# Kernel tuning notes

Hardware: AMD Instinct MI355X
Metric: run time of the kernel (lower is better)

Reference implementation:

```python
import jax, jax.numpy as jnp
import numpy as np

G = 8          # grid_size
DH = 32        # dim_head
EPS = 1e-5
INIT_LS = 1e-5


def setup_inputs() -> dict:
    key = jax.random.key(0)
    ks = jax.random.split(key, 8)
    B, H, W, C = 16, 128, 128, 256
    s = 1.0 / np.sqrt(C)
    return {
        "x": jax.random.normal(ks[0], (B, H, W, C), dtype=jnp.float32),
        "ln_w": jnp.ones((C,), jnp.float32),
        "ln_b": jnp.zeros((C,), jnp.float32),
        "in_proj_w": jax.random.uniform(ks[1], (3 * C, C), jnp.float32, -s, s),
        "in_proj_b": jnp.zeros((3 * C,), jnp.float32),
        "out_proj_w": jax.random.uniform(ks[2], (C, C), jnp.float32, -s, s),
        "out_proj_b": jnp.zeros((C,), jnp.float32),
        "gamma": jnp.full((C,), INIT_LS, jnp.float32),
    }


def _grid_attention(x, ln_w, ln_b, in_proj_w, in_proj_b, out_proj_w, out_proj_b, gamma):
    B, H, W, C = x.shape
    nh = C // DH
    # LayerNorm over channels
    mu = jnp.mean(x, axis=-1, keepdims=True)
    var = jnp.mean(jnp.square(x - mu), axis=-1, keepdims=True)
    x = (x - mu) * jax.lax.rsqrt(var + EPS) * ln_w + ln_b
    # grid partition: (B,G,H/G,G,W/G,C) -> (B,H/G,W/G,G,G,C) -> (N, G*G, C)
    hg, wg = H // G, W // G
    xw = x.reshape(B, G, hg, G, wg, C).transpose(0, 2, 4, 1, 3, 5)
    xw = xw.reshape(B * hg * wg, G * G, C)  # N windows of L=G*G tokens
    # MHSA (nn.MultiheadAttention semantics)
    qkv = xw @ in_proj_w.T + in_proj_b                      # (N, L, 3C)
    q, k, v = jnp.split(qkv, 3, axis=-1)
    N, L = xw.shape[0], xw.shape[1]
    q = q.reshape(N, L, nh, DH).transpose(0, 2, 1, 3)        # (N, nh, L, DH)
    k = k.reshape(N, L, nh, DH).transpose(0, 2, 1, 3)
    v = v.reshape(N, L, nh, DH).transpose(0, 2, 1, 3)
    scores = jnp.einsum("nhld,nhmd->nhlm", q, k) / np.sqrt(DH)
    attn = jax.nn.softmax(scores, axis=-1)
    out = jnp.einsum("nhlm,nhmd->nhld", attn, v)             # (N, nh, L, DH)
    out = out.transpose(0, 2, 1, 3).reshape(N, L, C)
    out = out @ out_proj_w.T + out_proj_b
    # LayerScale
    out = out * gamma
    # grid reverse: (B,H/G,W/G,G,G,C) -> (B,G,H/G,G,W/G,C) -> (B,H,W,C)
    out = out.reshape(B, hg, wg, G, G, C).transpose(0, 3, 1, 4, 2, 5)
    return out.reshape(B, H, W, C)


def reference(x, ln_w, ln_b, in_proj_w, in_proj_b, out_proj_w, out_proj_b, gamma):
    return _grid_attention(x, ln_w, ln_b, in_proj_w, in_proj_b,
                           out_proj_w, out_proj_b, gamma)
```

## Files before the change

kernel.cpp:

```cpp
#include <hip/hip_runtime.h>
#include <hip/hip_bf16.h>

typedef __attribute__((ext_vector_type(8))) short short8;
typedef __attribute__((ext_vector_type(4))) float f32x4;
typedef __attribute__((ext_vector_type(4))) unsigned short us4;
typedef __attribute__((ext_vector_type(2))) unsigned uint2v;

union U8 { unsigned u[4]; short8 s; };

__device__ __forceinline__ unsigned short f2b(float f) {
  unsigned u = __float_as_uint(f);
  u += 0x7FFFu + ((u >> 16) & 1u);
  return (unsigned short)(u >> 16);
}
__device__ __forceinline__ float b2f(unsigned short h) {
  return __uint_as_float((unsigned)h << 16);
}
__device__ __forceinline__ unsigned pkbf(float lo, float hi) {
  __hip_bfloat162 h = __float22bfloat162_rn(make_float2(lo, hi));
  unsigned u; __builtin_memcpy(&u, &h, 4);
  return u;
}
__device__ __forceinline__ void swp32(unsigned &a, unsigned &b) {
#if __has_builtin(__builtin_amdgcn_permlane32_swap)
  uint2v r = __builtin_amdgcn_permlane32_swap(a, b, false, false);
  a = r.x; b = r.y;
#else
  asm volatile("v_permlane32_swap_b32 %0, %1" : "+v"(a), "+v"(b));
#endif
}
__device__ __forceinline__ void swp16(unsigned &a, unsigned &b) {
#if __has_builtin(__builtin_amdgcn_permlane16_swap)
  uint2v r = __builtin_amdgcn_permlane16_swap(a, b, false, false);
  a = r.x; b = r.y;
#else
  asm volatile("v_permlane16_swap_b32 %0, %1" : "+v"(a), "+v"(b));
#endif
}

__global__ __launch_bounds__(64) void prep(
    const float* __restrict__ wq, const float* __restrict__ wo,
    const float* __restrict__ lnw, const float* __restrict__ lnb,
    const float* __restrict__ bqkv, const float* __restrict__ bo,
    const float* __restrict__ gm,
    unsigned short* __restrict__ wbf, float* __restrict__ Sarr,
    float* __restrict__ Carr, float* __restrict__ boG) {
  int d = blockIdx.x, lane = threadIdx.x;
  if (d < 768) {
    float4 wv = *(const float4*)(wq + (size_t)d * 256 + lane * 4);
    float4 lw = *(const float4*)(lnw + lane * 4);
    float4 lb = *(const float4*)(lnb + lane * 4);
    us4 o;
    o.x = f2b(wv.x * lw.x); o.y = f2b(wv.y * lw.y);
    o.z = f2b(wv.z * lw.z); o.w = f2b(wv.w * lw.w);
    *(us4*)(wbf + (size_t)d * 256 + lane * 4) = o;
    float s = b2f(o.x) + b2f(o.y) + b2f(o.z) + b2f(o.w);
    float c = wv.x * lb.x + wv.y * lb.y + wv.z * lb.z + wv.w * lb.w;
    #pragma unroll
    for (int m = 32; m >= 1; m >>= 1) { s += __shfl_xor(s, m); c += __shfl_xor(c, m); }
    if (lane == 0) { Sarr[d] = s; Carr[d] = c + bqkv[d]; }
  } else {
    int dd = d - 768;
    float g = gm[dd];
    float4 wv = *(const float4*)(wo + (size_t)dd * 256 + lane * 4);
    us4 o;
    o.x = f2b(wv.x * g); o.y = f2b(wv.y * g); o.z = f2b(wv.z * g); o.w = f2b(wv.w * g);
    *(us4*)(wbf + 196608 + (size_t)dd * 256 + lane * 4) = o;
    if (lane == 0) boG[dd] = bo[dd] * g;
  }
}

__global__ __launch_bounds__(512, 4) void grid_attn(
    const float* __restrict__ x,
    const unsigned short* __restrict__ Wqkv,
    const unsigned short* __restrict__ Wout,
    const float* __restrict__ Sarr,
    const float* __restrict__ Carr,
    const float* __restrict__ boG,
    float* __restrict__ out) {

  __shared__ unsigned short ldsX[64 * 264];
  __shared__ float ldsMu[64];
  __shared__ float ldsRs[64];

  const int tid = threadIdx.x;
  const int w   = tid >> 6;
  const int lid = tid & 63;
  const int l16 = lid & 15;
  const int lhi = lid >> 4;

  const int n  = blockIdx.x;
  const int b  = n >> 8;
  const int wi = (n >> 4) & 15;
  const int wj = n & 15;

  {
    float2 p[8];
    #pragma unroll
    for (int t = 0; t < 8; ++t) {
      int l = w * 8 + t;
      int a = l >> 3, cg = l & 7;
      int hh = a * 16 + wi, ww = cg * 16 + wj;
      float4 v = *(const float4*)(x + ((size_t)((b * 128 + hh) * 128 + ww)) * 256 + lid * 4);
      p[t].x = v.x + v.y + v.z + v.w;
      p[t].y = v.x * v.x + v.y * v.y + v.z * v.z + v.w * v.w;
      uint2v o; o.x = pkbf(v.x, v.y); o.y = pkbf(v.z, v.w);
      *(uint2v*)(&ldsX[l * 264 + lid * 4]) = o;
    }
    const int h1 = lid & 1, h2 = (lid >> 1) & 1, h4 = (lid >> 2) & 1;
    float2 q[4];
    #pragma unroll
    for (int i = 0; i < 4; ++i) {
      float sx = h1 ? p[i].x : p[i + 4].x, sy = h1 ? p[i].y : p[i + 4].y;
      float kx = h1 ? p[i + 4].x : p[i].x, ky = h1 ? p[i + 4].y : p[i].y;
      q[i].x = kx + __shfl_xor(sx, 1);
      q[i].y = ky + __shfl_xor(sy, 1);
    }
    float2 r2[2];
    #pragma unroll
    for (int i = 0; i < 2; ++i) {
      float sx = h2 ? q[i].x : q[i + 2].x, sy = h2 ? q[i].y : q[i + 2].y;
      float kx = h2 ? q[i + 2].x : q[i].x, ky = h2 ? q[i + 2].y : q[i].y;
      r2[i].x = kx + __shfl_xor(sx, 2);
      r2[i].y = ky + __shfl_xor(sy, 2);
    }
    float fx, fy;
    {
      float sx = h4 ? r2[0].x : r2[1].x, sy = h4 ? r2[0].y : r2[1].y;
      float kx = h4 ? r2[1].x : r2[0].x, ky = h4 ? r2[1].y : r2[0].y;
      fx = kx + __shfl_xor(sx, 4);
      fy = ky + __shfl_xor(sy, 4);
    }
    fx += __shfl_xor(fx, 8);  fy += __shfl_xor(fy, 8);
    fx += __shfl_xor(fx, 16); fy += __shfl_xor(fy, 16);
    fx += __shfl_xor(fx, 32); fy += __shfl_xor(fy, 32);
    if (lid < 8) {
      int T = h1 * 4 + h2 * 2 + h4;
      float mu = fx * (1.0f / 256.0f);
      float var = fy * (1.0f / 256.0f) - mu * mu;
      ldsMu[w * 8 + T] = mu;
      ldsRs[w * 8 + T] = rsqrtf(var + 1e-5f);
    }
  }
  __syncthreads();

  short8 vtf[2][2];
  {
    f32x4 va[4][2];
    #pragma unroll
    for (int tt = 0; tt < 4; ++tt)
      #pragma unroll
      for (int dt = 0; dt < 2; ++dt)
        va[tt][dt] = (f32x4){0.f, 0.f, 0.f, 0.f};
    const unsigned short* wvp = Wqkv + (size_t)(512 + w * 32 + l16) * 256 + lhi * 8;
    #pragma unroll 4
    for (int kc = 0; kc < 8; ++kc) {
      short8 wv0 = *(const short8*)(wvp + kc * 32);
      short8 wv1 = *(const short8*)(wvp + 16 * 256 + kc * 32);
      #pragma unroll
      for (int tt = 0; tt < 4; ++tt) {
        short8 xf = *(const short8*)(&ldsX[(tt * 16 + l16) * 264 + kc * 32 + lhi * 8]);
        va[tt][0] = __builtin_amdgcn_mfma_f32_16x16x32_bf16(xf, wv0, va[tt][0], 0, 0, 0);
        va[tt][1] = __builtin_amdgcn_mfma_f32_16x16x32_bf16(xf, wv1, va[tt][1], 0, 0, 0);
      }
    }
    #pragma unroll
    for (int dt = 0; dt < 2; ++dt) {
      float Sv = Sarr[512 + w * 32 + dt * 16 + l16];
      float Cv = Carr[512 + w * 32 + dt * 16 + l16];
      unsigned bu[8];
      #pragma unroll
      for (int tt = 0; tt < 4; ++tt) {
        f32x4 rs4 = *(const f32x4*)(&ldsRs[tt * 16 + lhi * 4]);
        f32x4 m4  = *(const f32x4*)(&ldsMu[tt * 16 + lhi * 4]);
        float v0 = fmaf(rs4[0], fmaf(-m4[0], Sv, va[tt][dt][0]), Cv);
        float v1 = fmaf(rs4[1], fmaf(-m4[1], Sv, va[tt][dt][1]), Cv);
        float v2 = fmaf(rs4[2], fmaf(-m4[2], Sv, va[tt][dt][2]), Cv);
        float v3 = fmaf(rs4[3], fmaf(-m4[3], Sv, va[tt][dt][3]), Cv);
        bu[tt * 2]     = pkbf(v0, v1);
        bu[tt * 2 + 1] = pkbf(v2, v3);
      }
      swp32(bu[0], bu[2]); swp32(bu[1], bu[3]); swp32(bu[4], bu[6]); swp32(bu[5], bu[7]);
      swp16(bu[0], bu[2]); swp16(bu[1], bu[3]); swp16(bu[4], bu[6]); swp16(bu[5], bu[7]);
      U8 z0, z1;
      z0.u[0] = bu[0]; z0.u[1] = bu[1]; z0.u[2] = bu[2]; z0.u[3] = bu[3];
      z1.u[0] = bu[4]; z1.u[1] = bu[5]; z1.u[2] = bu[6]; z1.u[3] = bu[7];
      vtf[dt][0] = z0.s;
      vtf[dt][1] = z1.s;
    }
  }

  short8 qf[4], kf[4];

  {
    f32x4 qa[2][4];
    #pragma unroll
    for (int dt = 0; dt < 2; ++dt)
      #pragma unroll
      for (int tt = 0; tt < 4; ++tt)
        qa[dt][tt] = (f32x4){0.f, 0.f, 0.f, 0.f};
    const unsigned short* wqp = Wqkv + (size_t)(w * 32 + l16) * 256 + lhi * 8;
    #pragma unroll 4
    for (int kc = 0; kc < 8; ++kc) {
      short8 wq0 = *(const short8*)(wqp + kc * 32);
      short8 wq1 = *(const short8*)(wqp + 16 * 256 + kc * 32);
      #pragma unroll
      for (int tt = 0; tt < 4; ++tt) {
        short8 xf = *(const short8*)(&ldsX[(tt * 16 + l16) * 264 + kc * 32 + lhi * 8]);
        qa[0][tt] = __builtin_amdgcn_mfma_f32_16x16x32_bf16(wq0, xf, qa[0][tt], 0, 0, 0);
        qa[1][tt] = __builtin_amdgcn_mfma_f32_16x16x32_bf16(wq1, xf, qa[1][tt], 0, 0, 0);
      }
    }
    f32x4 S0 = *(const f32x4*)(Sarr + w * 32 + lhi * 4);
    f32x4 S1 = *(const f32x4*)(Sarr + w * 32 + 16 + lhi * 4);
    f32x4 C0 = *(const f32x4*)(Carr + w * 32 + lhi * 4);
    f32x4 C1 = *(const f32x4*)(Carr + w * 32 + 16 + lhi * 4);
    #pragma unroll
    for (int tt = 0; tt < 4; ++tt) {
      float rs  = ldsRs[tt * 16 + l16];
      float nmu = -ldsMu[tt * 16 + l16];
      float e0[4], e1[4];
      #pragma unroll
      for (int r = 0; r < 4; ++r) {
        e0[r] = fmaf(rs, fmaf(nmu, S0[r], qa[0][tt][r]), C0[r]);
        e1[r] = fmaf(rs, fmaf(nmu, S1[r], qa[1][tt][r]), C1[r]);
      }
      unsigned a0 = pkbf(e0[0], e0[1]), a1 = pkbf(e0[2], e0[3]);
      unsigned a2 = pkbf(e1[0], e1[1]), a3 = pkbf(e1[2], e1[3]);
      swp32(a0, a2); swp32(a1, a3);
      swp16(a0, a2); swp16(a1, a3);
      U8 z; z.u[0] = a0; z.u[1] = a1; z.u[2] = a2; z.u[3] = a3;
      qf[tt] = z.s;
    }
  }

  {
    f32x4 ka[2][4];
    #pragma unroll
    for (int dt = 0; dt < 2; ++dt)
      #pragma unroll
      for (int tt = 0; tt < 4; ++tt)
        ka[dt][tt] = (f32x4){0.f, 0.f, 0.f, 0.f};
    const unsigned short* wkp = Wqkv + (size_t)(256 + w * 32 + l16) * 256 + lhi * 8;
    #pragma unroll 4
    for (int kc = 0; kc < 8; ++kc) {
      short8 wk0 = *(const short8*)(wkp + kc * 32);
      short8 wk1 = *(const short8*)(wkp + 16 * 256 + kc * 32);
      #pragma unroll
      for (int tt = 0; tt < 4; ++tt) {
        short8 xf = *(const short8*)(&ldsX[(tt * 16 + l16) * 264 + kc * 32 + lhi * 8]);
        ka[0][tt] = __builtin_amdgcn_mfma_f32_16x16x32_bf16(wk0, xf, ka[0][tt], 0, 0, 0);
        ka[1][tt] = __builtin_amdgcn_mfma_f32_16x16x32_bf16(wk1, xf, ka[1][tt], 0, 0, 0);
      }
    }
    f32x4 S0 = *(const f32x4*)(Sarr + 256 + w * 32 + lhi * 4);
    f32x4 S1 = *(const f32x4*)(Sarr + 256 + w * 32 + 16 + lhi * 4);
    f32x4 C0 = *(const f32x4*)(Carr + 256 + w * 32 + lhi * 4);
    f32x4 C1 = *(const f32x4*)(Carr + 256 + w * 32 + 16 + lhi * 4);
    #pragma unroll
    for (int tt = 0; tt < 4; ++tt) {
      float rs  = ldsRs[tt * 16 + l16];
      float nmu = -ldsMu[tt * 16 + l16];
      float e0[4], e1[4];
      #pragma unroll
      for (int r = 0; r < 4; ++r) {
        e0[r] = fmaf(rs, fmaf(nmu, S0[r], ka[0][tt][r]), C0[r]);
        e1[r] = fmaf(rs, fmaf(nmu, S1[r], ka[1][tt][r]), C1[r]);
      }
      unsigned a0 = pkbf(e0[0], e0[1]), a1 = pkbf(e0[2], e0[3]);
      unsigned a2 = pkbf(e1[0], e1[1]), a3 = pkbf(e1[2], e1[3]);
      swp32(a0, a2); swp32(a1, a3);
      swp16(a0, a2); swp16(a1, a3);
      U8 z; z.u[0] = a0; z.u[1] = a1; z.u[2] = a2; z.u[3] = a3;
      kf[tt] = z.s;
    }
  }

  uint2v po[4][2];
  const float K2 = 0.25503487013594137f;
  #pragma unroll
  for (int nn = 0; nn < 4; ++nn) {
    f32x4 s[4];
    #pragma unroll
    for (int m = 0; m < 4; ++m)
      s[m] = __builtin_amdgcn_mfma_f32_16x16x32_bf16(kf[m], qf[nn], (f32x4){0.f,0.f,0.f,0.f}, 0, 0, 0);
    float mx = s[0][0];
    #pragma unroll
    for (int m = 0; m < 4; ++m)
      #pragma unroll
      for (int r = 0; r < 4; ++r)
        mx = fmaxf(mx, s[m][r]);
    mx = fmaxf(mx, __shfl_xor(mx, 16));
    mx = fmaxf(mx, __shfl_xor(mx, 32));
    float sum = 0.f;
    unsigned bu[8];
    #pragma unroll
    for (int m = 0; m < 4; ++m) {
      float e0 = exp2f((s[m][0] - mx) * K2);
      float e1 = exp2f((s[m][1] - mx) * K2);
      float e2 = exp2f((s[m][2] - mx) * K2);
      float e3 = exp2f((s[m][3] - mx) * K2);
      sum += (e0 + e1) + (e2 + e3);
      bu[m * 2]     = pkbf(e0, e1);
      bu[m * 2 + 1] = pkbf(e2, e3);
    }
    sum += __shfl_xor(sum, 16);
    sum += __shfl_xor(sum, 32);
    float iv = 1.0f / sum;
    swp32(bu[0], bu[2]); swp32(bu[1], bu[3]); swp32(bu[4], bu[6]); swp32(bu[5], bu[7]);
    swp16(bu[0], bu[2]); swp16(bu[1], bu[3]); swp16(bu[4], bu[6]); swp16(bu[5], bu[7]);
    U8 z0, z1;
    z0.u[0] = bu[0]; z0.u[1] = bu[1]; z0.u[2] = bu[2]; z0.u[3] = bu[3];
    z1.u[0] = bu[4]; z1.u[1] = bu[5]; z1.u[2] = bu[6]; z1.u[3] = bu[7];
    f32x4 ot0 = (f32x4){0.f,0.f,0.f,0.f};
    f32x4 ot1 = (f32x4){0.f,0.f,0.f,0.f};
    ot0 = __builtin_amdgcn_mfma_f32_16x16x32_bf16(vtf[0][0], z0.s, ot0, 0, 0, 0);
    ot0 = __builtin_amdgcn_mfma_f32_16x16x32_bf16(vtf[0][1], z1.s, ot0, 0, 0, 0);
    ot1 = __builtin_amdgcn_mfma_f32_16x16x32_bf16(vtf[1][0], z0.s, ot1, 0, 0, 0);
    ot1 = __builtin_amdgcn_mfma_f32_16x16x32_bf16(vtf[1][1], z1.s, ot1, 0, 0, 0);
    po[nn][0].x = pkbf(ot0[0] * iv, ot0[1] * iv);
    po[nn][0].y = pkbf(ot0[2] * iv, ot0[3] * iv);
    po[nn][1].x = pkbf(ot1[0] * iv, ot1[1] * iv);
    po[nn][1].y = pkbf(ot1[2] * iv, ot1[3] * iv);
  }

  __syncthreads();

  #pragma unroll
  for (int nn = 0; nn < 4; ++nn)
    #pragma unroll
    for (int dt = 0; dt < 2; ++dt)
      *(uint2v*)(&ldsX[(nn * 16 + l16) * 264 + w * 32 + dt * 16 + lhi * 4]) = po[nn][dt];
  __syncthreads();

  f32x4 ya[4][2];
  #pragma unroll
  for (int mt = 0; mt < 4; ++mt)
    #pragma unroll
    for (int nt = 0; nt < 2; ++nt)
      ya[mt][nt] = (f32x4){0.f, 0.f, 0.f, 0.f};
  {
    const unsigned short* wop = Wout + (size_t)(w * 32 + l16) * 256 + lhi * 8;
    #pragma unroll 4
    for (int kc = 0; kc < 8; ++kc) {
      short8 wf0 = *(const short8*)(wop + kc * 32);
      short8 wf1 = *(const short8*)(wop + 16 * 256 + kc * 32);
      #pragma unroll
      for (int mt = 0; mt < 4; ++mt) {
        short8 af = *(const short8*)(&ldsX[(mt * 16 + l16) * 264 + kc * 32 + lhi * 8]);
        ya[mt][0] = __builtin_amdgcn_mfma_f32_16x16x32_bf16(af, wf0, ya[mt][0], 0, 0, 0);
        ya[mt][1] = __builtin_amdgcn_mfma_f32_16x16x32_bf16(af, wf1, ya[mt][1], 0, 0, 0);
      }
    }
  }

  float ob0 = boG[w * 32 + l16];
  float ob1 = boG[w * 32 + 16 + l16];
  #pragma unroll
  for (int mt = 0; mt < 4; ++mt)
    #pragma unroll
    for (int r = 0; r < 4; ++r) {
      int row = mt * 16 + lhi * 4 + r;
      int a = row >> 3, cg = row & 7;
      int hh = a * 16 + wi, ww2 = cg * 16 + wj;
      float* pout = out + ((size_t)((b * 128 + hh) * 128 + ww2)) * 256 + w * 32;
      pout[l16]      = ya[mt][0][r] + ob0;
      pout[l16 + 16] = ya[mt][1][r] + ob1;
    }
}

extern "C" void kernel_launch(void* const* d_in, const int* in_sizes, int n_in,
                              void* d_out, int out_size, void* d_ws, size_t ws_size,
                              hipStream_t stream) {
  const float* x    = (const float*)d_in[0];
  const float* ln_w = (const float*)d_in[1];
  const float* ln_b = (const float*)d_in[2];
  const float* ipw  = (const float*)d_in[3];
  const float* ipb  = (const float*)d_in[4];
  const float* opw  = (const float*)d_in[5];
  const float* opb  = (const float*)d_in[6];
  const float* gm   = (const float*)d_in[7];

  unsigned short* wbf = (unsigned short*)d_ws;
  float* Sarr = (float*)(wbf + 262144);
  float* Carr = Sarr + 768;
  float* boG  = Carr + 768;

  prep<<<1024, 64, 0, stream>>>(ipw, opw, ln_w, ln_b, ipb, opb, gm,
                                wbf, Sarr, Carr, boG);
  grid_attn<<<4096, 512, 0, stream>>>(x, wbf, wbf + 196608,
                                      Sarr, Carr, boG, (float*)d_out);
}
```

Before: 352.0 us.

## Apply LayerNorm before bf16 staging and seed QKV accumulators with bias

Instead of folding the LayerNorm affine into the weights and correcting each projection output with per-row mu/rstd terms, the kernel now normalizes x in registers (using ln_w/ln_b) before packing to bf16 in LDS. QKV accumulators are initialized with the in-proj bias, which removes the per-output epilogue FMAs and the S/C side arrays from the prep kernel. It also replaces shfl_xor cross-row reductions with permlane16/32 swap based reductions in LN stats and softmax. The trade-off is that the eight float4 x loads stay live in registers until the stats are ready, which raises register pressure, and precision changes slightly.

```diff
diff --git a/kernel.cpp b/kernel.cpp
--- a/kernel.cpp
+++ b/kernel.cpp
@@ -13,52 +13,46 @@
   u += 0x7FFFu + ((u >> 16) & 1u);
   return (unsigned short)(u >> 16);
 }
-__device__ __forceinline__ float b2f(unsigned short h) {
-  return __uint_as_float((unsigned)h << 16);
-}
 __device__ __forceinline__ unsigned pkbf(float lo, float hi) {
   __hip_bfloat162 h = __float22bfloat162_rn(make_float2(lo, hi));
   unsigned u; __builtin_memcpy(&u, &h, 4);
   return u;
 }
 __device__ __forceinline__ void swp32(unsigned &a, unsigned &b) {
-#if __has_builtin(__builtin_amdgcn_permlane32_swap)
   uint2v r = __builtin_amdgcn_permlane32_swap(a, b, false, false);
   a = r.x; b = r.y;
-#else
-  asm volatile("v_permlane32_swap_b32 %0, %1" : "+v"(a), "+v"(b));
-#endif
 }
 __device__ __forceinline__ void swp16(unsigned &a, unsigned &b) {
-#if __has_builtin(__builtin_amdgcn_permlane16_swap)
   uint2v r = __builtin_amdgcn_permlane16_swap(a, b, false, false);
   a = r.x; b = r.y;
-#else
-  asm volatile("v_permlane16_swap_b32 %0, %1" : "+v"(a), "+v"(b));
-#endif
+}
+__device__ __forceinline__ float redq_max(float v) {
+  uint2v r = __builtin_amdgcn_permlane16_swap(__float_as_uint(v), __float_as_uint(v), false, false);
+  v = fmaxf(__uint_as_float(r.x), __uint_as_float(r.y));
+  r = __builtin_amdgcn_permlane32_swap(__float_as_uint(v), __float_as_uint(v), false, false);
+  return fmaxf(__uint_as_float(r.x), __uint_as_float(r.y));
+}
+__device__ __forceinline__ float redq_sum(float v) {
+  uint2v r = __builtin_amdgcn_permlane16_swap(__float_as_uint(v), __float_as_uint(v), false, false);
+  v = __uint_as_float(r.x) + __uint_as_float(r.y);
+  r = __builtin_amdgcn_permlane32_swap(__float_as_uint(v), __float_as_uint(v), false, false);
+  return __uint_as_float(r.x) + __uint_as_float(r.y);
+}
+__device__ __forceinline__ float red5_sum(float v) {
+  v += __shfl_xor(v, 8);
+  return redq_sum(v);
 }
 
 __global__ __launch_bounds__(64) void prep(
     const float* __restrict__ wq, const float* __restrict__ wo,
-    const float* __restrict__ lnw, const float* __restrict__ lnb,
-    const float* __restrict__ bqkv, const float* __restrict__ bo,
-    const float* __restrict__ gm,
-    unsigned short* __restrict__ wbf, float* __restrict__ Sarr,
-    float* __restrict__ Carr, float* __restrict__ boG) {
+    const float* __restrict__ gm, const float* __restrict__ bo,
+    unsigned short* __restrict__ wbf, float* __restrict__ boG) {
   int d = blockIdx.x, lane = threadIdx.x;
   if (d < 768) {
     float4 wv = *(const float4*)(wq + (size_t)d * 256 + lane * 4);
-    float4 lw = *(const float4*)(lnw + lane * 4);
-    float4 lb = *(const float4*)(lnb + lane * 4);
     us4 o;
-    o.x = f2b(wv.x * lw.x); o.y = f2b(wv.y * lw.y);
-    o.z = f2b(wv.z * lw.z); o.w = f2b(wv.w * lw.w);
+    o.x = f2b(wv.x); o.y = f2b(wv.y); o.z = f2b(wv.z); o.w = f2b(wv.w);
     *(us4*)(wbf + (size_t)d * 256 + lane * 4) = o;
-    float s = b2f(o.x) + b2f(o.y) + b2f(o.z) + b2f(o.w);
-    float c = wv.x * lb.x + wv.y * lb.y + wv.z * lb.z + wv.w * lb.w;
-    #pragma unroll
-    for (int m = 32; m >= 1; m >>= 1) { s += __shfl_xor(s, m); c += __shfl_xor(c, m); }
-    if (lane == 0) { Sarr[d] = s; Carr[d] = c + bqkv[d]; }
   } else {
     int dd = d - 768;
     float g = gm[dd];
@@ -72,10 +66,11 @@
 
 __global__ __launch_bounds__(512, 4) void grid_attn(
     const float* __restrict__ x,
+    const float* __restrict__ lnw4,
+    const float* __restrict__ lnb4,
     const unsigned short* __restrict__ Wqkv,
+    const float* __restrict__ bqkv,
     const unsigned short* __restrict__ Wout,
-    const float* __restrict__ Sarr,
-    const float* __restrict__ Carr,
     const float* __restrict__ boG,
     float* __restrict__ out) {
 
@@ -95,17 +90,16 @@
   const int wj = n & 15;
 
   {
+    float4 v[8];
     float2 p[8];
     #pragma unroll
     for (int t = 0; t < 8; ++t) {
       int l = w * 8 + t;
       int a = l >> 3, cg = l & 7;
       int hh = a * 16 + wi, ww = cg * 16 + wj;
-      float4 v = *(const float4*)(x + ((size_t)((b * 128 + hh) * 128 + ww)) * 256 + lid * 4);
-      p[t].x = v.x + v.y + v.z + v.w;
-      p[t].y = v.x * v.x + v.y * v.y + v.z * v.z + v.w * v.w;
-      uint2v o; o.x = pkbf(v.x, v.y); o.y = pkbf(v.z, v.w);
-      *(uint2v*)(&ldsX[l * 264 + lid * 4]) = o;
+      v[t] = *(const float4*)(x + ((size_t)((b * 128 + hh) * 128 + ww)) * 256 + lid * 4);
+      p[t].x = v[t].x + v[t].y + v[t].z + v[t].w;
+      p[t].y = v[t].x * v[t].x + v[t].y * v[t].y + v[t].z * v[t].z + v[t].w * v[t].w;
     }
     const int h1 = lid & 1, h2 = (lid >> 1) & 1, h4 = (lid >> 2) & 1;
     float2 q[4];
@@ -131,9 +125,8 @@
       fx = kx + __shfl_xor(sx, 4);
       fy = ky + __shfl_xor(sy, 4);
     }
-    fx += __shfl_xor(fx, 8);  fy += __shfl_xor(fy, 8);
-    fx += __shfl_xor(fx, 16); fy += __shfl_xor(fy, 16);
-    fx += __shfl_xor(fx, 32); fy += __shfl_xor(fy, 32);
+    fx = red5_sum(fx);
+    fy = red5_sum(fy);
     if (lid < 8) {
       int T = h1 * 4 + h2 * 2 + h4;
       float mu = fx * (1.0f / 256.0f);
@@ -141,17 +134,33 @@
       ldsMu[w * 8 + T] = mu;
       ldsRs[w * 8 + T] = rsqrtf(var + 1e-5f);
     }
+    float4 lw = *(const float4*)(lnw4 + lid * 4);
+    float4 lb = *(const float4*)(lnb4 + lid * 4);
+    #pragma unroll
+    for (int t = 0; t < 8; ++t) {
+      int l = w * 8 + t;
+      float mu = ldsMu[w * 8 + t];
+      float rs = ldsRs[w * 8 + t];
+      float n0 = (v[t].x - mu) * rs * lw.x + lb.x;
+      float n1 = (v[t].y - mu) * rs * lw.y + lb.y;
+      float n2 = (v[t].z - mu) * rs * lw.z + lb.z;
+      float n3 = (v[t].w - mu) * rs * lw.w + lb.w;
+      uint2v o; o.x = pkbf(n0, n1); o.y = pkbf(n2, n3);
+      *(uint2v*)(&ldsX[l * 264 + lid * 4]) = o;
+    }
   }
   __syncthreads();
 
   short8 vtf[2][2];
   {
+    float bv0 = bqkv[512 + w * 32 + l16];
+    float bv1 = bqkv[512 + w * 32 + 16 + l16];
     f32x4 va[4][2];
     #pragma unroll
-    for (int tt = 0; tt < 4; ++tt)
-      #pragma unroll
-      for (int dt = 0; dt < 2; ++dt)
-        va[tt][dt] = (f32x4){0.f, 0.f, 0.f, 0.f};
+    for (int tt = 0; tt < 4; ++tt) {
+      va[tt][0] = (f32x4){bv0, bv0, bv0, bv0};
+      va[tt][1] = (f32x4){bv1, bv1, bv1, bv1};
+    }
     const unsigned short* wvp = Wqkv + (size_t)(512 + w * 32 + l16) * 256 + lhi * 8;
     #pragma unroll 4
     for (int kc = 0; kc < 8; ++kc) {
@@ -166,19 +175,11 @@
     }
     #pragma unroll
     for (int dt = 0; dt < 2; ++dt) {
-      float Sv = Sarr[512 + w * 32 + dt * 16 + l16];
-      float Cv = Carr[512 + w * 32 + dt * 16 + l16];
       unsigned bu[8];
       #pragma unroll
       for (int tt = 0; tt < 4; ++tt) {
-        f32x4 rs4 = *(const f32x4*)(&ldsRs[tt * 16 + lhi * 4]);
-        f32x4 m4  = *(const f32x4*)(&ldsMu[tt * 16 + lhi * 4]);
-        float v0 = fmaf(rs4[0], fmaf(-m4[0], Sv, va[tt][dt][0]), Cv);
-        float v1 = fmaf(rs4[1], fmaf(-m4[1], Sv, va[tt][dt][1]), Cv);
-        float v2 = fmaf(rs4[2], fmaf(-m4[2], Sv, va[tt][dt][2]), Cv);
-        float v3 = fmaf(rs4[3], fmaf(-m4[3], Sv, va[tt][dt][3]), Cv);
-        bu[tt * 2]     = pkbf(v0, v1);
-        bu[tt * 2 + 1] = pkbf(v2, v3);
+        bu[tt * 2]     = pkbf(va[tt][dt][0], va[tt][dt][1]);
+        bu[tt * 2 + 1] = pkbf(va[tt][dt][2], va[tt][dt][3]);
       }
       swp32(bu[0], bu[2]); swp32(bu[1], bu[3]); swp32(bu[4], bu[6]); swp32(bu[5], bu[7]);
       swp16(bu[0], bu[2]); swp16(bu[1], bu[3]); swp16(bu[4], bu[6]); swp16(bu[5], bu[7]);
@@ -193,12 +194,11 @@
   short8 qf[4], kf[4];
 
   {
+    f32x4 Cq0 = *(const f32x4*)(bqkv + w * 32 + lhi * 4);
+    f32x4 Cq1 = *(const f32x4*)(bqkv + w * 32 + 16 + lhi * 4);
     f32x4 qa[2][4];
     #pragma unroll
-    for (int dt = 0; dt < 2; ++dt)
-      #pragma unroll
-      for (int tt = 0; tt < 4; ++tt)
-        qa[dt][tt] = (f32x4){0.f, 0.f, 0.f, 0.f};
+    for (int tt = 0; tt < 4; ++tt) { qa[0][tt] = Cq0; qa[1][tt] = Cq1; }
     const unsigned short* wqp = Wqkv + (size_t)(w * 32 + l16) * 256 + lhi * 8;
     #pragma unroll 4
     for (int kc = 0; kc < 8; ++kc) {
@@ -211,22 +211,10 @@
         qa[1][tt] = __builtin_amdgcn_mfma_f32_16x16x32_bf16(wq1, xf, qa[1][tt], 0, 0, 0);
       }
     }
-    f32x4 S0 = *(const f32x4*)(Sarr + w * 32 + lhi * 4);
-    f32x4 S1 = *(const f32x4*)(Sarr + w * 32 + 16 + lhi * 4);
-    f32x4 C0 = *(const f32x4*)(Carr + w * 32 + lhi * 4);
-    f32x4 C1 = *(const f32x4*)(Carr + w * 32 + 16 + lhi * 4);
     #pragma unroll
     for (int tt = 0; tt < 4; ++tt) {
-      float rs  = ldsRs[tt * 16 + l16];
-      float nmu = -ldsMu[tt * 16 + l16];
-      float e0[4], e1[4];
-      #pragma unroll
-      for (int r = 0; r < 4; ++r) {
-        e0[r] = fmaf(rs, fmaf(nmu, S0[r], qa[0][tt][r]), C0[r]);
-        e1[r] = fmaf(rs, fmaf(nmu, S1[r], qa[1][tt][r]), C1[r]);
-      }
-      unsigned a0 = pkbf(e0[0], e0[1]), a1 = pkbf(e0[2], e0[3]);
-      unsigned a2 = pkbf(e1[0], e1[1]), a3 = pkbf(e1[2], e1[3]);
+      unsigned a0 = pkbf(qa[0][tt][0], qa[0][tt][1]), a1 = pkbf(qa[0][tt][2], qa[0][tt][3]);
+      unsigned a2 = pkbf(qa[1][tt][0], qa[1][tt][1]), a3 = pkbf(qa[1][tt][2], qa[1][tt][3]);
       swp32(a0, a2); swp32(a1, a3);
       swp16(a0, a2); swp16(a1, a3);
       U8 z; z.u[0] = a0; z.u[1] = a1; z.u[2] = a2; z.u[3] = a3;
@@ -235,12 +223,11 @@
   }
 
   {
+    f32x4 Ck0 = *(const f32x4*)(bqkv + 256 + w * 32 + lhi * 4);
+    f32x4 Ck1 = *(const f32x4*)(bqkv + 256 + w * 32 + 16 + lhi * 4);
     f32x4 ka[2][4];
     #pragma unroll
-    for (int dt = 0; dt < 2; ++dt)
-      #pragma unroll
-      for (int tt = 0; tt < 4; ++tt)
-        ka[dt][tt] = (f32x4){0.f, 0.f, 0.f, 0.f};
+    for (int tt = 0; tt < 4; ++tt) { ka[0][tt] = Ck0; ka[1][tt] = Ck1; }
     const unsigned short* wkp = Wqkv + (size_t)(256 + w * 32 + l16) * 256 + lhi * 8;
     #pragma unroll 4
     for (int kc = 0; kc < 8; ++kc) {
@@ -253,22 +240,10 @@
         ka[1][tt] = __builtin_amdgcn_mfma_f32_16x16x32_bf16(wk1, xf, ka[1][tt], 0, 0, 0);
       }
     }
-    f32x4 S0 = *(const f32x4*)(Sarr + 256 + w * 32 + lhi * 4);
-    f32x4 S1 = *(const f32x4*)(Sarr + 256 + w * 32 + 16 + lhi * 4);
-    f32x4 C0 = *(const f32x4*)(Carr + 256 + w * 32 + lhi * 4);
-    f32x4 C1 = *(const f32x4*)(Carr + 256 + w * 32 + 16 + lhi * 4);
     #pragma unroll
     for (int tt = 0; tt < 4; ++tt) {
-      float rs  = ldsRs[tt * 16 + l16];
-      float nmu = -ldsMu[tt * 16 + l16];
-      float e0[4], e1[4];
-      #pragma unroll
-      for (int r = 0; r < 4; ++r) {
-        e0[r] = fmaf(rs, fmaf(nmu, S0[r], ka[0][tt][r]), C0[r]);
-        e1[r] = fmaf(rs, fmaf(nmu, S1[r], ka[1][tt][r]), C1[r]);
-      }
-      unsigned a0 = pkbf(e0[0], e0[1]), a1 = pkbf(e0[2], e0[3]);
-      unsigned a2 = pkbf(e1[0], e1[1]), a3 = pkbf(e1[2], e1[3]);
+      unsigned a0 = pkbf(ka[0][tt][0], ka[0][tt][1]), a1 = pkbf(ka[0][tt][2], ka[0][tt][3]);
+      unsigned a2 = pkbf(ka[1][tt][0], ka[1][tt][1]), a3 = pkbf(ka[1][tt][2], ka[1][tt][3]);
       swp32(a0, a2); swp32(a1, a3);
       swp16(a0, a2); swp16(a1, a3);
       U8 z; z.u[0] = a0; z.u[1] = a1; z.u[2] = a2; z.u[3] = a3;
@@ -284,15 +259,13 @@
     #pragma unroll
     for (int m = 0; m < 4; ++m)
       s[m] = __builtin_amdgcn_mfma_f32_16x16x32_bf16(kf[m], qf[nn], (f32x4){0.f,0.f,0.f,0.f}, 0, 0, 0);
-    float mx = s[0][0];
+    float mm[4];
     #pragma unroll
     for (int m = 0; m < 4; ++m)
-      #pragma unroll
-      for (int r = 0; r < 4; ++r)
-        mx = fmaxf(mx, s[m][r]);
-    mx = fmaxf(mx, __shfl_xor(mx, 16));
-    mx = fmaxf(mx, __shfl_xor(mx, 32));
-    float sum = 0.f;
+      mm[m] = fmaxf(fmaxf(s[m][0], s[m][1]), fmaxf(s[m][2], s[m][3]));
+    float mx = fmaxf(fmaxf(mm[0], mm[1]), fmaxf(mm[2], mm[3]));
+    mx = redq_max(mx);
+    float sm[4];
     unsigned bu[8];
     #pragma unroll
     for (int m = 0; m < 4; ++m) {
@@ -300,12 +273,12 @@
       float e1 = exp2f((s[m][1] - mx) * K2);
       float e2 = exp2f((s[m][2] - mx) * K2);
       float e3 = exp2f((s[m][3] - mx) * K2);
-      sum += (e0 + e1) + (e2 + e3);
+      sm[m] = (e0 + e1) + (e2 + e3);
       bu[m * 2]     = pkbf(e0, e1);
       bu[m * 2 + 1] = pkbf(e2, e3);
     }
-    sum += __shfl_xor(sum, 16);
-    sum += __shfl_xor(sum, 32);
+    float sum = (sm[0] + sm[1]) + (sm[2] + sm[3]);
+    sum = redq_sum(sum);
     float iv = 1.0f / sum;
     swp32(bu[0], bu[2]); swp32(bu[1], bu[3]); swp32(bu[4], bu[6]); swp32(bu[5], bu[7]);
     swp16(bu[0], bu[2]); swp16(bu[1], bu[3]); swp16(bu[4], bu[6]); swp16(bu[5], bu[7]);
@@ -382,12 +355,9 @@
   const float* gm   = (const float*)d_in[7];
 
   unsigned short* wbf = (unsigned short*)d_ws;
-  float* Sarr = (float*)(wbf + 262144);
-  float* Carr = Sarr + 768;
-  float* boG  = Carr + 768;
-
-  prep<<<1024, 64, 0, stream>>>(ipw, opw, ln_w, ln_b, ipb, opb, gm,
-                                wbf, Sarr, Carr, boG);
-  grid_attn<<<4096, 512, 0, stream>>>(x, wbf, wbf + 196608,
-                                      Sarr, Carr, boG, (float*)d_out);
-}
+  float* boG = (float*)(wbf + 262144);
+
+  prep<<<1024, 64, 0, stream>>>(ipw, opw, gm, opb, wbf, boG);
+  grid_attn<<<4096, 512, 0, stream>>>(x, ln_w, ln_b, wbf, ipb,
+                                      wbf + 196608, boG, (float*)d_out);
+}
```

Result: faster. 344.3 us (-2.2%).
